# Kernel tuning notes

Measured on AMD Instinct MI355X. Metric: run time of the kernel, lower is better.

## Reference

```python
import jax, jax.numpy as jnp
import numpy as np

SUB = 8          # Config.sub_sampling
CROP = 24        # max feature-space ROI extent given proposal generator
NEG = jnp.float32(-1e30)


def _roi_adaptive_maxpool(feature_map, coords):
    """Vectorized equivalent of the per-proposal tf.slice + AdaptivePooling((2,2)) loop.
    feature_map: [1,H,W,C]; coords: [N,4] int (y0,x0,y1,x1) in image space.
    Returns [N,2,2,C]."""
    fm = feature_map[0]
    H, W, C = fm.shape
    sy = jnp.minimum(coords[:, 0] // SUB, H - 2)              # min(coord0//8, 74)
    sx = jnp.minimum(coords[:, 1] // SUB, W - 2)              # min(coord1//8, 126)
    ey = (coords[:, 2] + SUB - 1) // SUB                      # ceil(coord2/8)
    ex = (coords[:, 3] + SUB - 1) // SUB                      # ceil(coord3/8)
    h = jnp.maximum(ey - sy, 2)                               # max(end-start, 2)
    w = jnp.maximum(ex - sx, 2)
    # fixed-size crop per proposal (padding keeps dynamic_slice in-bounds; pad area masked out)
    fm_pad = jnp.pad(fm, ((0, CROP), (0, CROP), (0, 0)))
    crop = jax.vmap(lambda y, x: jax.lax.dynamic_slice(fm_pad, (y, x, 0), (CROP, CROP, C)))(sy, sx)
    # adaptive 2-bin boundaries: bin i covers [floor(i*s/2), ceil((i+1)*s/2))
    idx = jnp.arange(CROP)
    two = jnp.arange(2)

    def bin_mask(size):                                        # size [N] -> [N,2,CROP]
        start = (two[None, :] * size[:, None]) // 2
        end = ((two[None, :] + 1) * size[:, None] + 1) // 2
        return (idx[None, None, :] >= start[:, :, None]) & (idx[None, None, :] < end[:, :, None])

    rmask = bin_mask(h)                                        # [N,2,CROP]
    cmask = bin_mask(w)                                        # [N,2,CROP]
    # separable masked max: rows first, then cols
    m1 = jnp.where(rmask[:, :, :, None, None], crop[:, None], NEG)   # [N,2,CROP,CROP,C]
    t = m1.max(axis=2)                                               # [N,2,CROP,C]
    m2 = jnp.where(cmask[:, None, :, :, None], t[:, :, None], NEG)   # [N,2,2,CROP,C]
    return m2.max(axis=3)                                            # [N,2,2,C]


def setup_inputs() -> dict:
    key = jax.random.key(0)
    ks = jax.random.split(key, 12)
    N, C = 256, 512
    feature_map = jax.random.normal(ks[0], (1, 76, 128, C), jnp.float32)
    y0 = jax.random.randint(ks[1], (N,), 0, 584)
    x0 = jax.random.randint(ks[2], (N,), 0, 1000)
    hh = jax.random.randint(ks[3], (N,), 16, 176)
    ww = jax.random.randint(ks[4], (N,), 16, 176)
    y1 = jnp.minimum(y0 + hh, 607)
    x1 = jnp.minimum(x0 + ww, 1023)
    proposal_coords = jnp.stack([y0, x0, y1, x1], axis=1).astype(jnp.int32)
    s = 0.02
    return {
        'feature_map': feature_map,
        'proposal_coords': proposal_coords,
        'W1': s * jax.random.normal(ks[5], (2 * 2 * C, 200), jnp.float32),
        'b1': jnp.zeros((200,), jnp.float32),
        'W2': s * jax.random.normal(ks[6], (200, 200), jnp.float32),
        'b2': jnp.zeros((200,), jnp.float32),
        'W3': s * jax.random.normal(ks[7], (200, 16), jnp.float32),
        'b3': jnp.zeros((16,), jnp.float32),
        'W4': s * jax.random.normal(ks[8], (200, 5), jnp.float32),
        'b4': jnp.zeros((5,), jnp.float32),
    }


def reference(feature_map, proposal_coords, W1, b1, W2, b2, W3, b3, W4, b4):
    coords = proposal_coords.astype(jnp.int32)
    pooled = _roi_adaptive_maxpool(feature_map, coords)        # [N,2,2,C]
    N = pooled.shape[0]
    f = pooled.reshape(N, -1)
    f = jax.nn.relu(f @ W1 + b1)
    f = jax.nn.relu(f @ W2 + b2)
    pred_reg = (f @ W3 + b3).reshape(N, 4, 4)
    pred_cls = f @ W4 + b4                                     # [N,5]
    cls = jnp.argmax(pred_cls, axis=1)
    probs = jax.nn.softmax(pred_cls, axis=1)
    scores = probs[:, 1:].max(axis=1)
    # per-proposal reg deltas for the predicted class (bg uses clipped index; masked out below)
    reg = jnp.take_along_axis(pred_reg, jnp.maximum(cls - 1, 0)[:, None, None], axis=1)[:, 0]  # [N,4]
    pc = coords.astype(jnp.float32)
    ph = pc[:, 2] - pc[:, 0]
    pw = pc[:, 3] - pc[:, 1]
    py = pc[:, 0] + 0.5 * ph
    px = pc[:, 1] + 0.5 * pw
    p_y = ph * reg[:, 0] + py
    p_x = pw * reg[:, 1] + px
    p_h = ph * jnp.clip(jnp.exp(reg[:, 2]), 0.001, 20.0)
    p_w = pw * jnp.clip(jnp.exp(reg[:, 3]), 0.001, 20.0)
    boxes = jnp.stack([p_y, p_x, p_h, p_w], axis=1)            # [N,4]
    non_bg_mask = cls != 0                                     # fixed-shape stand-in for np.where filtering
    return boxes, scores, non_bg_mask
```

## Files before the change

kernel.cpp:

```cpp
#include <hip/hip_runtime.h>
#include <math.h>

#define CCH 512
#define FH 76
#define FW 128
#define NP 256
#define HID 200
#define NKC 16
#define FM4 (FH * FW * (CCH / 4))
#define PG_THREADS (512 * 512)

__global__ __launch_bounds__(512) void poolgemm_kernel(
    const float4* __restrict__ fm4, const int* __restrict__ coords,
    const float* __restrict__ W1, float* __restrict__ part,
    float* __restrict__ scratch)
{
    __shared__ float4 sm[2][8][32];
    __shared__ float  fsub[8][128];
    __shared__ float  pc[2][8][HID];

    const int t   = threadIdx.x;
    const int r0  = blockIdx.x * 8;
    const int kc  = blockIdx.y;
    const int bin = kc >> 2;
    const int cb  = (kc & 3) * 32;
    const int k0  = kc * 128;

    {
        const int gtid = (blockIdx.y * 32 + blockIdx.x) * 512 + t;
        float wacc = -1e30f;
        #pragma unroll
        for (int i = 0; i < 5; ++i) {
            const int idx = gtid + i * PG_THREADS;
            if (idx < FM4) {
                const float4 v = fm4[idx];
                wacc = fmaxf(wacc, fmaxf(fmaxf(v.x, v.y), fmaxf(v.z, v.w)));
            }
        }
        if (gtid < 102400) {
            const float4 v = ((const float4*)W1)[gtid];
            wacc = fmaxf(wacc, fmaxf(fmaxf(v.x, v.y), fmaxf(v.z, v.w)));
        }
        if (wacc > 1e29f) scratch[0] = wacc;
    }

    {
        const int rslot = t >> 8;
        const int nl    = (t >> 5) & 7;
        const int cg    = t & 31;
        const int n  = r0 + nl;
        const int c0 = coords[n*4+0], c1 = coords[n*4+1];
        const int c2 = coords[n*4+2], c3 = coords[n*4+3];
        const int sy = min(c0 >> 3, FH - 2);
        const int sx = min(c1 >> 3, FW - 2);
        const int h = max(((c2 + 7) >> 3) - sy, 2);
        const int w = max(((c3 + 7) >> 3) - sx, 2);
        const int by = bin >> 1, bx = bin & 1;
        const int rs = by ? (h >> 1) : 0;
        const int re = by ? h : ((h + 1) >> 1);
        const int cs = bx ? (w >> 1) : 0;
        const int ce = bx ? w : ((w + 1) >> 1);
        const int nc = ce - cs;
        float4 m = make_float4(-1e30f, -1e30f, -1e30f, -1e30f);
        for (int r = rs + rslot; r < re; r += 2) {
            const float4* row = fm4 +
                ((size_t)(sy + r) * FW + sx + cs) * (CCH/4) + cb + cg;
            #pragma unroll 4
            for (int cc = 0; cc < nc; ++cc) {
                const float4 v = row[(size_t)cc * (CCH/4)];
                m.x = fmaxf(m.x, v.x); m.y = fmaxf(m.y, v.y);
                m.z = fmaxf(m.z, v.z); m.w = fmaxf(m.w, v.w);
            }
        }
        sm[rslot][nl][cg] = m;
    }
    __syncthreads();
    if (t < 256) {
        const int nl = t >> 5, cg = t & 31;
        const float4 a = sm[0][nl][cg], b = sm[1][nl][cg];
        float4 o;
        o.x = fmaxf(a.x, b.x); o.y = fmaxf(a.y, b.y);
        o.z = fmaxf(a.z, b.z); o.w = fmaxf(a.w, b.w);
        *((float4*)&fsub[nl][cg * 4]) = o;
    }
    __syncthreads();

    {
        const int half = t >> 8;
        const int j    = t & 255;
        if (j < HID) {
            float acc[8];
            #pragma unroll
            for (int r = 0; r < 8; ++r) acc[r] = 0.0f;
            const int kk0 = half * 64;
            const float* wp = W1 + (size_t)(k0 + kk0) * HID + j;
            #pragma unroll 8
            for (int kk = 0; kk < 64; ++kk) {
                const float wv = wp[(size_t)kk * HID];
                #pragma unroll
                for (int r = 0; r < 8; ++r)
                    acc[r] += fsub[r][kk0 + kk] * wv;
            }
            #pragma unroll
            for (int r = 0; r < 8; ++r) pc[half][r][j] = acc[r];
        }
    }
    __syncthreads();
    if (t < HID) {
        float* pp = part + ((size_t)kc * NP + r0) * HID + t;
        #pragma unroll
        for (int r = 0; r < 8; ++r)
            pp[(size_t)r * HID] = pc[0][r][t] + pc[1][r][t];
    }
}

__global__ __launch_bounds__(512) void head_kernel(
    const float* __restrict__ part,
    const float* __restrict__ b1, const float* __restrict__ W2,
    const float* __restrict__ b2, const float* __restrict__ W3,
    const float* __restrict__ b3, const float* __restrict__ W4,
    const float* __restrict__ b4, const int* __restrict__ coords,
    float* __restrict__ out)
{
    __shared__ float h1s[HID];
    __shared__ float h2s[HID];
    __shared__ float p2[2][HID];
    __shared__ float hdp[2][21];
    __shared__ float hd[21];
    const int n = blockIdx.x;
    const int t = threadIdx.x;
    const int kc = t >> 8;
    const int j  = t & 255;
    if (t < HID) {
        float a = b1[t];
        #pragma unroll
        for (int c = 0; c < NKC; ++c)
            a += part[((size_t)c * NP + n) * HID + t];
        h1s[t] = fmaxf(a, 0.0f);
    }
    __syncthreads();
    if (j < HID) {
        const int k0 = kc * 100;
        float acc = 0.0f;
        #pragma unroll 10
        for (int k = 0; k < 100; ++k)
            acc += h1s[k0 + k] * W2[(k0 + k) * HID + j];
        p2[kc][j] = acc;
    }
    __syncthreads();
    if (t < HID) h2s[t] = fmaxf(p2[0][t] + p2[1][t] + b2[t], 0.0f);
    __syncthreads();
    if (j < 21) {
        const int k0 = kc * 100;
        float acc = 0.0f;
        if (j < 16) {
            #pragma unroll 5
            for (int k = 0; k < 100; ++k)
                acc += h2s[k0 + k] * W3[(k0 + k) * 16 + j];
        } else {
            const int ci = j - 16;
            #pragma unroll 5
            for (int k = 0; k < 100; ++k)
                acc += h2s[k0 + k] * W4[(k0 + k) * 5 + ci];
        }
        hdp[kc][j] = acc;
    }
    __syncthreads();
    if (t < 21)
        hd[t] = hdp[0][t] + hdp[1][t] + (t < 16 ? b3[t] : b4[t - 16]);
    __syncthreads();
    if (t == 0) {
        const float cv0 = hd[16], cv1 = hd[17], cv2 = hd[18],
                    cv3 = hd[19], cv4 = hd[20];
        int cls = 0; float best = cv0;
        if (cv1 > best) { best = cv1; cls = 1; }
        if (cv2 > best) { best = cv2; cls = 2; }
        if (cv3 > best) { best = cv3; cls = 3; }
        if (cv4 > best) { best = cv4; cls = 4; }
        const float e0 = expf(cv0 - best), e1 = expf(cv1 - best),
                    e2 = expf(cv2 - best), e3 = expf(cv3 - best),
                    e4 = expf(cv4 - best);
        const float s = e0 + e1 + e2 + e3 + e4;
        const float score = fmaxf(fmaxf(e1, e2), fmaxf(e3, e4)) / s;
        const int ri = max(cls - 1, 0);
        const float rg0 = hd[ri*4+0], rg1 = hd[ri*4+1],
                    rg2 = hd[ri*4+2], rg3 = hd[ri*4+3];
        const float y0 = (float)coords[n*4+0], x0 = (float)coords[n*4+1];
        const float y1 = (float)coords[n*4+2], x1 = (float)coords[n*4+3];
        const float ph = y1 - y0, pw = x1 - x0;
        const float py = y0 + 0.5f * ph, px = x0 + 0.5f * pw;
        const float oy = ph * rg0 + py;
        const float ox = pw * rg1 + px;
        const float oh = ph * fminf(fmaxf(expf(rg2), 0.001f), 20.0f);
        const float ow = pw * fminf(fmaxf(expf(rg3), 0.001f), 20.0f);
        out[n*4+0] = oy; out[n*4+1] = ox; out[n*4+2] = oh; out[n*4+3] = ow;
        out[NP*4 + n] = score;
        out[NP*5 + n] = (cls != 0) ? 1.0f : 0.0f;
    }
}

extern "C" void kernel_launch(void* const* d_in, const int* in_sizes, int n_in,
                              void* d_out, int out_size, void* d_ws, size_t ws_size,
                              hipStream_t stream) {
    const float* fm     = (const float*)d_in[0];
    const int*   coords = (const int*)  d_in[1];
    const float* W1 = (const float*)d_in[2];
    const float* b1 = (const float*)d_in[3];
    const float* W2 = (const float*)d_in[4];
    const float* b2 = (const float*)d_in[5];
    const float* W3 = (const float*)d_in[6];
    const float* b3 = (const float*)d_in[7];
    const float* W4 = (const float*)d_in[8];
    const float* b4 = (const float*)d_in[9];
    float* out = (float*)d_out;

    float* part    = (float*)d_ws;
    float* scratch = part + (size_t)NKC * NP * HID;

    poolgemm_kernel<<<dim3(32, NKC), 512, 0, stream>>>(
        (const float4*)fm, coords, W1, part, scratch);
    head_kernel<<<NP, 512, 0, stream>>>(part, b1, W2, b2, W3, b3, W4, b4,
                                        coords, out);
}
```

Baseline: 120.4 us.

## Fuse MLP head into pool-GEMM kernel via last-block-arrives counter

Merges the two kernels into one. Each row-tile keeps an atomic arrival counter, and the last of the 16 K-chunk blocks to finish reduces the partial sums and runs the fc2/fc3/fc4 head for its 8 proposals. The head now processes 8 rows per block, so W2 is reused across rows instead of being reloaded for every proposal. This removes a kernel launch and the per-proposal head blocks, at the cost of adding a memset, atomics and a serialized tail on only 32 winner blocks. The warm-up max pass is also extended to cover W2.

Measured after the change: 146.6 us. 21.7% more time.

```diff
diff --git a/kernel.cpp b/kernel.cpp
--- a/kernel.cpp
+++ b/kernel.cpp
@@ -7,17 +7,28 @@
 #define NP 256
 #define HID 200
 #define NKC 16
+#define NTILE 32
 #define FM4 (FH * FW * (CCH / 4))
 #define PG_THREADS (512 * 512)
 
-__global__ __launch_bounds__(512) void poolgemm_kernel(
+
+__global__ __launch_bounds__(512) void fused_kernel(
     const float4* __restrict__ fm4, const int* __restrict__ coords,
-    const float* __restrict__ W1, float* __restrict__ part,
-    float* __restrict__ scratch)
+    const float* __restrict__ W1, const float* __restrict__ b1,
+    const float* __restrict__ W2, const float* __restrict__ b2,
+    const float* __restrict__ W3, const float* __restrict__ b3,
+    const float* __restrict__ W4, const float* __restrict__ b4,
+    float* __restrict__ part, unsigned int* __restrict__ cnt,
+    float* __restrict__ scratch, float* __restrict__ out)
 {
     __shared__ float4 sm[2][8][32];
     __shared__ float  fsub[8][128];
     __shared__ float  pc[2][8][HID];
+    __shared__ float  pbuf[2][8][HID];
+    __shared__ float  hbuf[8][HID];
+    __shared__ float  hdp[2][8][21];
+    __shared__ float  hd[8][21];
+    __shared__ int    winner;
 
     const int t   = threadIdx.x;
     const int r0  = blockIdx.x * 8;
@@ -27,7 +38,7 @@
     const int k0  = kc * 128;
 
     {
-        const int gtid = (blockIdx.y * 32 + blockIdx.x) * 512 + t;
+        const int gtid = (blockIdx.y * NTILE + blockIdx.x) * 512 + t;
         float wacc = -1e30f;
         #pragma unroll
         for (int i = 0; i < 5; ++i) {
@@ -39,6 +50,10 @@
         }
         if (gtid < 102400) {
             const float4 v = ((const float4*)W1)[gtid];
+            wacc = fmaxf(wacc, fmaxf(fmaxf(v.x, v.y), fmaxf(v.z, v.w)));
+        }
+        if (gtid < 10000) {
+            const float4 v = ((const float4*)W2)[gtid];
             wacc = fmaxf(wacc, fmaxf(fmaxf(v.x, v.y), fmaxf(v.z, v.w)));
         }
         if (wacc > 1e29f) scratch[0] = wacc;
@@ -85,25 +100,23 @@
     }
     __syncthreads();
 
-    {
-        const int half = t >> 8;
-        const int j    = t & 255;
-        if (j < HID) {
-            float acc[8];
-            #pragma unroll
-            for (int r = 0; r < 8; ++r) acc[r] = 0.0f;
-            const int kk0 = half * 64;
-            const float* wp = W1 + (size_t)(k0 + kk0) * HID + j;
-            #pragma unroll 8
-            for (int kk = 0; kk < 64; ++kk) {
-                const float wv = wp[(size_t)kk * HID];
-                #pragma unroll
-                for (int r = 0; r < 8; ++r)
-                    acc[r] += fsub[r][kk0 + kk] * wv;
-            }
-            #pragma unroll
-            for (int r = 0; r < 8; ++r) pc[half][r][j] = acc[r];
-        }
+    const int half = t >> 8;
+    const int j    = t & 255;
+    if (j < HID) {
+        float acc[8];
+        #pragma unroll
+        for (int r = 0; r < 8; ++r) acc[r] = 0.0f;
+        const int kk0 = half * 64;
+        const float* wp = W1 + (size_t)(k0 + kk0) * HID + j;
+        #pragma unroll 8
+        for (int kk = 0; kk < 64; ++kk) {
+            const float wv = wp[(size_t)kk * HID];
+            #pragma unroll
+            for (int r = 0; r < 8; ++r)
+                acc[r] += fsub[r][kk0 + kk] * wv;
+        }
+        #pragma unroll
+        for (int r = 0; r < 8; ++r) pc[half][r][j] = acc[r];
     }
     __syncthreads();
     if (t < HID) {
@@ -112,66 +125,89 @@
         for (int r = 0; r < 8; ++r)
             pp[(size_t)r * HID] = pc[0][r][t] + pc[1][r][t];
     }
-}
-
-__global__ __launch_bounds__(512) void head_kernel(
-    const float* __restrict__ part,
-    const float* __restrict__ b1, const float* __restrict__ W2,
-    const float* __restrict__ b2, const float* __restrict__ W3,
-    const float* __restrict__ b3, const float* __restrict__ W4,
-    const float* __restrict__ b4, const int* __restrict__ coords,
-    float* __restrict__ out)
-{
-    __shared__ float h1s[HID];
-    __shared__ float h2s[HID];
-    __shared__ float p2[2][HID];
-    __shared__ float hdp[2][21];
-    __shared__ float hd[21];
-    const int n = blockIdx.x;
-    const int t = threadIdx.x;
-    const int kc = t >> 8;
-    const int j  = t & 255;
+    __syncthreads();
+
+    if (t == 0) {
+        __threadfence();
+        const unsigned int old = __hip_atomic_fetch_add(
+            &cnt[blockIdx.x * 32], 1u, __ATOMIC_ACQ_REL,
+            __HIP_MEMORY_SCOPE_AGENT);
+        winner = (old == NKC - 1);
+        if (winner) __threadfence();
+    }
+    __syncthreads();
+    if (!winner) return;
+
+    if (j < HID) {
+        float acc[8];
+        #pragma unroll
+        for (int r = 0; r < 8; ++r) acc[r] = 0.0f;
+        #pragma unroll
+        for (int c = 0; c < 8; ++c) {
+            const int kk = half * 8 + c;
+            #pragma unroll
+            for (int r = 0; r < 8; ++r)
+                acc[r] += part[((size_t)kk * NP + r0 + r) * HID + j];
+        }
+        #pragma unroll
+        for (int r = 0; r < 8; ++r) pbuf[half][r][j] = acc[r];
+    }
+    __syncthreads();
     if (t < HID) {
-        float a = b1[t];
-        #pragma unroll
-        for (int c = 0; c < NKC; ++c)
-            a += part[((size_t)c * NP + n) * HID + t];
-        h1s[t] = fmaxf(a, 0.0f);
+        #pragma unroll
+        for (int r = 0; r < 8; ++r)
+            hbuf[r][t] = fmaxf(pbuf[0][r][t] + pbuf[1][r][t] + b1[t], 0.0f);
     }
     __syncthreads();
     if (j < HID) {
-        const int k0 = kc * 100;
-        float acc = 0.0f;
-        #pragma unroll 10
-        for (int k = 0; k < 100; ++k)
-            acc += h1s[k0 + k] * W2[(k0 + k) * HID + j];
-        p2[kc][j] = acc;
-    }
-    __syncthreads();
-    if (t < HID) h2s[t] = fmaxf(p2[0][t] + p2[1][t] + b2[t], 0.0f);
+        float acc[8];
+        #pragma unroll
+        for (int r = 0; r < 8; ++r) acc[r] = 0.0f;
+        const int kk0 = half * 100;
+        #pragma unroll 4
+        for (int k = 0; k < 100; ++k) {
+            const float wv = W2[(kk0 + k) * HID + j];
+            #pragma unroll
+            for (int r = 0; r < 8; ++r)
+                acc[r] += hbuf[r][kk0 + k] * wv;
+        }
+        #pragma unroll
+        for (int r = 0; r < 8; ++r) pbuf[half][r][j] = acc[r];
+    }
+    __syncthreads();
+    if (t < HID) {
+        #pragma unroll
+        for (int r = 0; r < 8; ++r)
+            hbuf[r][t] = fmaxf(pbuf[0][r][t] + pbuf[1][r][t] + b2[t], 0.0f);
+    }
     __syncthreads();
     if (j < 21) {
-        const int k0 = kc * 100;
-        float acc = 0.0f;
-        if (j < 16) {
-            #pragma unroll 5
-            for (int k = 0; k < 100; ++k)
-                acc += h2s[k0 + k] * W3[(k0 + k) * 16 + j];
-        } else {
-            const int ci = j - 16;
-            #pragma unroll 5
-            for (int k = 0; k < 100; ++k)
-                acc += h2s[k0 + k] * W4[(k0 + k) * 5 + ci];
-        }
-        hdp[kc][j] = acc;
-    }
-    __syncthreads();
-    if (t < 21)
-        hd[t] = hdp[0][t] + hdp[1][t] + (t < 16 ? b3[t] : b4[t - 16]);
-    __syncthreads();
-    if (t == 0) {
-        const float cv0 = hd[16], cv1 = hd[17], cv2 = hd[18],
-                    cv3 = hd[19], cv4 = hd[20];
+        float acc[8];
+        #pragma unroll
+        for (int r = 0; r < 8; ++r) acc[r] = 0.0f;
+        const int kk0 = half * 100;
+        #pragma unroll 4
+        for (int k = 0; k < 100; ++k) {
+            const float wv = (j < 16) ? W3[(kk0 + k) * 16 + j]
+                                      : W4[(kk0 + k) * 5 + (j - 16)];
+            #pragma unroll
+            for (int r = 0; r < 8; ++r)
+                acc[r] += hbuf[r][kk0 + k] * wv;
+        }
+        #pragma unroll
+        for (int r = 0; r < 8; ++r) hdp[half][r][j] = acc[r];
+    }
+    __syncthreads();
+    if (t < 168) {
+        const int r = t / 21, jj = t % 21;
+        hd[r][jj] = hdp[0][r][jj] + hdp[1][r][jj]
+                  + (jj < 16 ? b3[jj] : b4[jj - 16]);
+    }
+    __syncthreads();
+    if (t < 8) {
+        const int n = r0 + t;
+        const float cv0 = hd[t][16], cv1 = hd[t][17], cv2 = hd[t][18],
+                    cv3 = hd[t][19], cv4 = hd[t][20];
         int cls = 0; float best = cv0;
         if (cv1 > best) { best = cv1; cls = 1; }
         if (cv2 > best) { best = cv2; cls = 2; }
@@ -183,8 +219,8 @@
         const float s = e0 + e1 + e2 + e3 + e4;
         const float score = fmaxf(fmaxf(e1, e2), fmaxf(e3, e4)) / s;
         const int ri = max(cls - 1, 0);
-        const float rg0 = hd[ri*4+0], rg1 = hd[ri*4+1],
-                    rg2 = hd[ri*4+2], rg3 = hd[ri*4+3];
+        const float rg0 = hd[t][ri*4+0], rg1 = hd[t][ri*4+1],
+                    rg2 = hd[t][ri*4+2], rg3 = hd[t][ri*4+3];
         const float y0 = (float)coords[n*4+0], x0 = (float)coords[n*4+1];
         const float y1 = (float)coords[n*4+2], x1 = (float)coords[n*4+3];
         const float ph = y1 - y0, pw = x1 - x0;
@@ -214,11 +250,12 @@
     const float* b4 = (const float*)d_in[9];
     float* out = (float*)d_out;
 
-    float* part    = (float*)d_ws;
-    float* scratch = part + (size_t)NKC * NP * HID;
-
-    poolgemm_kernel<<<dim3(32, NKC), 512, 0, stream>>>(
-        (const float4*)fm, coords, W1, part, scratch);
-    head_kernel<<<NP, 512, 0, stream>>>(part, b1, W2, b2, W3, b3, W4, b4,
-                                        coords, out);
+    float*        part    = (float*)d_ws;
+    unsigned int* cnt     = (unsigned int*)(part + (size_t)NKC * NP * HID);
+    float*        scratch = (float*)(cnt + NTILE * 32);
+
+    hipMemsetAsync(cnt, 0, NTILE * 32 * sizeof(unsigned int), stream);
+    fused_kernel<<<dim3(NTILE, NKC), 512, 0, stream>>>(
+        (const float4*)fm, coords, W1, b1, W2, b2, W3, b3, W4, b4,
+        part, cnt, scratch, out);
 }
```
